# Kernel tuning notes

Hardware: AMD Instinct MI355X
Metric: run time of the kernel (lower is better)

Reference implementation:

```python
import jax, jax.numpy as jnp
import numpy as np

EPS = 1e-08
NEG_WEIGHT = 0.5
B, D = 4096, 256


def setup_inputs() -> dict:
    key = jax.random.key(0)
    k1, k2 = jax.random.split(key)
    feature_a = jax.random.normal(k1, (B, D), dtype=jnp.float32)
    feature_b = jax.random.normal(k2, (B, D), dtype=jnp.float32)
    labels = jnp.ones((B,), dtype=jnp.float32)  # positive pairs on the diagonal block
    return {"feature_a": feature_a, "feature_b": feature_b, "labels": labels}


def reference(feature_a, feature_b, labels):
    b = feature_a.shape[0]
    num_neg = b - 1
    # Cosine via single GEMM instead of the torch repeat/cat loop.
    # torch.nn.CosineSimilarity: dot / max(||a||*||b||, eps)
    na = jnp.sqrt(jnp.sum(feature_a * feature_a, axis=1))  # [B]
    nb = jnp.sqrt(jnp.sum(feature_b * feature_b, axis=1))  # [B]
    dots = jnp.einsum('kd,jd->kj', feature_a, feature_b)   # [B,B] dots[k,j]=a_k.b_j
    # torch ordering: block s (shift), row k pairs a_k with b_{(k+s) % B}
    k = jnp.arange(b)
    s = jnp.arange(b)
    idx = (k[None, :] + s[:, None]) % b                    # [S,K]
    cos = dots[k[None, :], idx] / jnp.maximum(na[None, :] * nb[idx], EPS)  # [S,K]
    logits = ((cos + 1.0) * 0.5).reshape(-1)               # flatten s-major (matches torch cat order)
    labels_full = jnp.concatenate(
        [labels.reshape(-1), jnp.zeros((num_neg * b,), dtype=labels.dtype)])
    weight = jnp.concatenate(
        [jnp.ones((b,), dtype=logits.dtype),
         jnp.full((num_neg * b,), NEG_WEIGHT, dtype=logits.dtype)])
    # BCELoss(weight, reduction='sum') with torch's log clamp at -100
    log_p = jnp.maximum(jnp.log(logits), -100.0)
    log_1mp = jnp.maximum(jnp.log1p(-logits), -100.0)
    loss = -jnp.sum(weight * (labels_full * log_p + (1.0 - labels_full) * log_1mp))
    return (logits, loss)
```

## Files before the change

### kernel.cpp

```cpp
#include <hip/hip_runtime.h>
#include <stdint.h>

#define NB 4096
#define ND 256

typedef __attribute__((ext_vector_type(8))) short short8;
typedef __attribute__((ext_vector_type(4))) float f32x4;

__device__ __forceinline__ unsigned short f2bf(float f) {
    unsigned int u = __float_as_uint(f);
    u += 0x7FFFu + ((u >> 16) & 1u);
    return (unsigned short)(u >> 16);
}

__device__ __forceinline__ void gload16(const void* g, void* lds_uniform) {
    __builtin_amdgcn_global_load_lds(
        (const __attribute__((address_space(1))) void*)(uintptr_t)g,
        (__attribute__((address_space(3))) void*)(unsigned int)(uintptr_t)lds_uniform,
        16, 0, 0);
}

__global__ void __launch_bounds__(256) prep_kernel(
    const float* __restrict__ A, const float* __restrict__ Bf,
    unsigned short* __restrict__ Abf, unsigned short* __restrict__ Bbf,
    float* __restrict__ rna, float* __restrict__ rnb, float* __restrict__ lossws)
{
    if (blockIdx.x == 0 && threadIdx.x < 64) lossws[threadIdx.x << 5] = 0.0f;
    int gw   = (blockIdx.x * 256 + threadIdx.x) >> 6;
    int lane = threadIdx.x & 63;
    const float* src; unsigned short* dst; float* rn; int row;
    if (gw < NB) { src = A;  dst = Abf; rn = rna; row = gw; }
    else         { src = Bf; dst = Bbf; rn = rnb; row = gw - NB; }

    float4 v = reinterpret_cast<const float4*>(src + (size_t)row * ND)[lane];
    float ss = v.x * v.x + v.y * v.y + v.z * v.z + v.w * v.w;
    #pragma unroll
    for (int off = 32; off > 0; off >>= 1) ss += __shfl_down(ss, off);
    if (lane == 0) rn[row] = 1.0f / sqrtf(fmaxf(ss, 1e-30f));

    ushort4 u;
    u.x = f2bf(v.x); u.y = f2bf(v.y); u.z = f2bf(v.z); u.w = f2bf(v.w);
    reinterpret_cast<ushort4*>(dst + (size_t)row * ND)[lane] = u;
}

__global__ void __launch_bounds__(256, 6) gemm_kernel(
    const unsigned short* __restrict__ Abf, const unsigned short* __restrict__ Bbf,
    const float* __restrict__ rna, const float* __restrict__ rnb,
    const float* __restrict__ labels, float* __restrict__ out,
    float* __restrict__ lossws)
{
    __shared__ __align__(16) char smem[24576];

    const int tid = threadIdx.x;
    const int w = tid >> 6, lane = tid & 63;
    const int lane15 = lane & 15, lhi = lane >> 4;
    const int bk = blockIdx.x & 63, bs = blockIdx.x >> 6;
    const int k0 = bk << 6, s0 = bs << 6;
    const int j0 = (k0 + s0) & (NB - 1);

    f32x4 acc[5];
    #pragma unroll
    for (int r = 0; r < 5; ++r) acc[r] = (f32x4)0.0f;

    auto stage = [&](int kt, char* buf) {
        {
            int slot0 = w << 6;
            int slot  = slot0 + lane;
            int row   = slot >> 2;
            int sch   = (slot ^ (slot >> 2) ^ (slot >> 4)) & 3;
            gload16(Abf + (size_t)(k0 + row) * ND + (kt << 5) + (sch << 3), buf + slot0 * 16);
        }
        #pragma unroll
        for (int i = 0; i < 2; ++i) {
            int slot0 = (i << 8) + (w << 6);
            int slot  = slot0 + lane;
            int row   = slot >> 2;
            int srow  = (j0 + row) & (NB - 1);
            int sch   = (slot ^ (slot >> 2) ^ (slot >> 4)) & 3;
            gload16(Bbf + (size_t)srow * ND + (kt << 5) + (sch << 3), buf + 4096 + slot0 * 16);
        }
    };

    stage(0, smem);
    __syncthreads();

    for (int kt = 0; kt < 8; ++kt) {
        char* buf = smem + ((kt & 1) ? 12288 : 0);
        if (kt < 7) stage(kt + 1, smem + ((kt & 1) ? 0 : 12288));
        const int f = (lane15 ^ (lane15 >> 2)) & 3;
        short8 af;
        {
            int row = (w << 4) + lane15;
            af = *reinterpret_cast<const short8*>(buf + row * 64 + ((lhi ^ f) << 4));
        }
        #pragma unroll
        for (int r = 0; r < 5; ++r) {
            int brow = (w << 4) + (r << 4) + lane15;
            short8 bfr = *reinterpret_cast<const short8*>(buf + 4096 + brow * 64 + ((lhi ^ f) << 4));
            acc[r] = __builtin_amdgcn_mfma_f32_16x16x32_bf16(af, bfr, acc[r], 0, 0, 0);
        }
        __syncthreads();
    }

    float* dw      = reinterpret_cast<float*>(smem);
    float* rnb_lds = reinterpret_cast<float*>(smem + 16384);
    float* rna_lds = reinterpret_cast<float*>(smem + 16896);
    float* lpart   = reinterpret_cast<float*>(smem + 17152);

    if (tid < 128) rnb_lds[tid] = rnb[(j0 + tid) & (NB - 1)];
    if (tid < 64)  rna_lds[tid] = rna[k0 + tid];

    #pragma unroll
    for (int r = 0; r < 5; ++r)
        #pragma unroll
        for (int e = 0; e < 4; ++e) {
            int t = (r << 4) + lane15 - (lhi << 2) - e;
            if ((unsigned)t < 64u) {
                int kap = (w << 4) + (lhi << 2) + e;
                dw[(t << 6) + (kap ^ ((t & 7) << 2))] = acc[r][e];
            }
        }
    __syncthreads();

    const int trow = (w << 4) + (lane >> 2);
    const int g0 = lane & 3;
    const int s = s0 + trow;
    float lacc = 0.0f;
    #pragma unroll
    for (int i = 0; i < 4; ++i) {
        int lg = (i << 2) + g0;
        int pg = lg ^ (trow & 7);
        f32x4 d  = *reinterpret_cast<f32x4*>(dw + (trow << 6) + (pg << 2));
        f32x4 na = *reinterpret_cast<f32x4*>(rna_lds + (lg << 2));
        f32x4 x;
        #pragma unroll
        for (int e = 0; e < 4; ++e) {
            float rb = rnb_lds[(lg << 2) + e + trow];
            x[e] = fmaf(d[e] * na[e] * rb, 0.5f, 0.5f);
        }
        *reinterpret_cast<f32x4*>(out + (size_t)s * NB + k0 + (lg << 2)) = x;
        float l1p0 = fmaxf(__logf(1.0f - x[0]), -100.0f);
        float l1p1 = fmaxf(__logf(1.0f - x[1]), -100.0f);
        float l1p2 = fmaxf(__logf(1.0f - x[2]), -100.0f);
        float l1p3 = fmaxf(__logf(1.0f - x[3]), -100.0f);
        if (s == 0) {
            float l1pv[4] = {l1p0, l1p1, l1p2, l1p3};
            #pragma unroll
            for (int e = 0; e < 4; ++e) {
                float lab = labels[k0 + (lg << 2) + e];
                float lp  = fmaxf(__logf(x[e]), -100.0f);
                lacc += lab * lp + (1.0f - lab) * l1pv[e];
            }
        } else {
            lacc += 0.5f * (l1p0 + l1p1 + l1p2 + l1p3);
        }
    }

    #pragma unroll
    for (int off = 32; off > 0; off >>= 1) lacc += __shfl_down(lacc, off);
    if (lane == 0) lpart[w] = lacc;
    __syncthreads();
    if (tid == 0) {
        float tot = lpart[0] + lpart[1] + lpart[2] + lpart[3];
        atomicAdd(lossws + ((blockIdx.x & 63) << 5), -tot);
    }
}

__global__ void finalize_kernel(const float* __restrict__ lossws, float* __restrict__ out) {
    float s = 0.0f;
    for (int i = 0; i < 64; ++i) s += lossws[i << 5];
    out[(size_t)NB * NB] = s;
}

extern "C" void kernel_launch(void* const* d_in, const int* in_sizes, int n_in,
                              void* d_out, int out_size, void* d_ws, size_t ws_size,
                              hipStream_t stream) {
    (void)in_sizes; (void)n_in; (void)out_size; (void)ws_size;
    const float* A      = (const float*)d_in[0];
    const float* Bf     = (const float*)d_in[1];
    const float* labels = (const float*)d_in[2];
    float* out = (float*)d_out;

    char* ws = (char*)d_ws;
    unsigned short* Abf = (unsigned short*)ws;
    unsigned short* Bbf = (unsigned short*)(ws + (size_t)2 * 1024 * 1024);
    float* rna    = (float*)(ws + (size_t)4 * 1024 * 1024);
    float* rnb    = (float*)(ws + (size_t)4 * 1024 * 1024 + 16384);
    float* lossws = (float*)(ws + (size_t)4 * 1024 * 1024 + 32768);

    hipLaunchKernelGGL(prep_kernel, dim3(2048), dim3(256), 0, stream,
                       A, Bf, Abf, Bbf, rna, rnb, lossws);
    hipLaunchKernelGGL(gemm_kernel, dim3(4096), dim3(256), 0, stream,
                       Abf, Bbf, rna, rnb, labels, out, lossws);
    hipLaunchKernelGGL(finalize_kernel, dim3(1), dim3(1), 0, stream, lossws, out);
}
```

Baseline: 47.93 us.

## Pre-normalize rows in prep and load MFMA operands directly from global

The prep kernel now scales each row by its inverse norm before converting to bf16, so the GEMM epilogue no longer loads or multiplies by per-row norms. The GEMM drops the LDS double-buffered staging and instead has each wave read its MFMA fragments straight from global memory (L2). Each wave now computes a 32-row k slice, and each block covers 128 k columns, which halves the grid. The epilogue is rewritten with a new swizzled LDS transpose and a lane permutation. Normalizing before the bf16 rounding slightly changes numerics, and the direct global loads depend on cache hits rather than on explicit reuse through LDS.

```diff
diff --git a/kernel.cpp b/kernel.cpp
--- a/kernel.cpp
+++ b/kernel.cpp
@@ -13,141 +13,127 @@
     return (unsigned short)(u >> 16);
 }
 
-__device__ __forceinline__ void gload16(const void* g, void* lds_uniform) {
-    __builtin_amdgcn_global_load_lds(
-        (const __attribute__((address_space(1))) void*)(uintptr_t)g,
-        (__attribute__((address_space(3))) void*)(unsigned int)(uintptr_t)lds_uniform,
-        16, 0, 0);
-}
-
 __global__ void __launch_bounds__(256) prep_kernel(
     const float* __restrict__ A, const float* __restrict__ Bf,
     unsigned short* __restrict__ Abf, unsigned short* __restrict__ Bbf,
-    float* __restrict__ rna, float* __restrict__ rnb, float* __restrict__ lossws)
+    float* __restrict__ lossws)
 {
     if (blockIdx.x == 0 && threadIdx.x < 64) lossws[threadIdx.x << 5] = 0.0f;
     int gw   = (blockIdx.x * 256 + threadIdx.x) >> 6;
     int lane = threadIdx.x & 63;
-    const float* src; unsigned short* dst; float* rn; int row;
-    if (gw < NB) { src = A;  dst = Abf; rn = rna; row = gw; }
-    else         { src = Bf; dst = Bbf; rn = rnb; row = gw - NB; }
+    const float* src; unsigned short* dst; int row;
+    if (gw < NB) { src = A;  dst = Abf; row = gw; }
+    else         { src = Bf; dst = Bbf; row = gw - NB; }
 
     float4 v = reinterpret_cast<const float4*>(src + (size_t)row * ND)[lane];
     float ss = v.x * v.x + v.y * v.y + v.z * v.z + v.w * v.w;
     #pragma unroll
-    for (int off = 32; off > 0; off >>= 1) ss += __shfl_down(ss, off);
-    if (lane == 0) rn[row] = 1.0f / sqrtf(fmaxf(ss, 1e-30f));
+    for (int off = 1; off < 64; off <<= 1) ss += __shfl_xor(ss, off);
+    float rn = 1.0f / sqrtf(fmaxf(ss, 1e-30f));
 
     ushort4 u;
-    u.x = f2bf(v.x); u.y = f2bf(v.y); u.z = f2bf(v.z); u.w = f2bf(v.w);
+    u.x = f2bf(v.x * rn); u.y = f2bf(v.y * rn);
+    u.z = f2bf(v.z * rn); u.w = f2bf(v.w * rn);
     reinterpret_cast<ushort4*>(dst + (size_t)row * ND)[lane] = u;
 }
 
-__global__ void __launch_bounds__(256, 6) gemm_kernel(
+__global__ void __launch_bounds__(256, 4) gemm_kernel(
     const unsigned short* __restrict__ Abf, const unsigned short* __restrict__ Bbf,
-    const float* __restrict__ rna, const float* __restrict__ rnb,
     const float* __restrict__ labels, float* __restrict__ out,
     float* __restrict__ lossws)
 {
-    __shared__ __align__(16) char smem[24576];
+    __shared__ __align__(16) float dw[64 * 128];
+    __shared__ float lpart[4];
 
     const int tid = threadIdx.x;
     const int w = tid >> 6, lane = tid & 63;
     const int lane15 = lane & 15, lhi = lane >> 4;
-    const int bk = blockIdx.x & 63, bs = blockIdx.x >> 6;
-    const int k0 = bk << 6, s0 = bs << 6;
-    const int j0 = (k0 + s0) & (NB - 1);
+    const int bk = blockIdx.x & 31, bs = blockIdx.x >> 5;
+    const int k0 = bk << 7, s0 = bs << 6;
+    const int kw = k0 + (w << 5);
 
-    f32x4 acc[5];
+    const short8* aptr[2];
+    const short8* bptr[6];
     #pragma unroll
-    for (int r = 0; r < 5; ++r) acc[r] = (f32x4)0.0f;
+    for (int m = 0; m < 2; ++m)
+        aptr[m] = reinterpret_cast<const short8*>(
+            Abf + (size_t)(kw + (m << 4) + lane15) * ND) + lhi;
+    #pragma unroll
+    for (int jf = 0; jf < 6; ++jf) {
+        int row = (kw + s0 + (jf << 4) + lane15) & (NB - 1);
+        bptr[jf] = reinterpret_cast<const short8*>(
+            Bbf + (size_t)row * ND) + lhi;
+    }
 
-    auto stage = [&](int kt, char* buf) {
-        {
-            int slot0 = w << 6;
-            int slot  = slot0 + lane;
-            int row   = slot >> 2;
-            int sch   = (slot ^ (slot >> 2) ^ (slot >> 4)) & 3;
-            gload16(Abf + (size_t)(k0 + row) * ND + (kt << 5) + (sch << 3), buf + slot0 * 16);
-        }
+    f32x4 acc[2][5];
+    #pragma unroll
+    for (int m = 0; m < 2; ++m)
         #pragma unroll
-        for (int i = 0; i < 2; ++i) {
-            int slot0 = (i << 8) + (w << 6);
-            int slot  = slot0 + lane;
-            int row   = slot >> 2;
-            int srow  = (j0 + row) & (NB - 1);
-            int sch   = (slot ^ (slot >> 2) ^ (slot >> 4)) & 3;
-            gload16(Bbf + (size_t)srow * ND + (kt << 5) + (sch << 3), buf + 4096 + slot0 * 16);
-        }
-    };
+        for (int r = 0; r < 5; ++r) acc[m][r] = (f32x4)0.0f;
 
-    stage(0, smem);
+    #pragma unroll
+    for (int ks = 0; ks < 8; ++ks) {
+        short8 a[2], b[6];
+        #pragma unroll
+        for (int m = 0; m < 2; ++m) a[m] = aptr[m][ks << 2];
+        #pragma unroll
+        for (int jf = 0; jf < 6; ++jf) b[jf] = bptr[jf][ks << 2];
+        #pragma unroll
+        for (int m = 0; m < 2; ++m)
+            #pragma unroll
+            for (int r = 0; r < 5; ++r)
+                acc[m][r] = __builtin_amdgcn_mfma_f32_16x16x32_bf16(
+                    a[m], b[m + r], acc[m][r], 0, 0, 0);
+    }
+
+    #pragma unroll
+    for (int m = 0; m < 2; ++m)
+        #pragma unroll
+        for (int r = 0; r < 5; ++r)
+            #pragma unroll
+            for (int e = 0; e < 4; ++e) {
+                int t = (r << 4) + lane15 - (lhi << 2) - e;
+                if ((unsigned)t < 64u) {
+                    int kap = (w << 5) + (m << 4) + (lhi << 2) + e;
+                    dw[(t << 7) + (kap ^ (t & 31))] = acc[m][r][e];
+                }
+            }
     __syncthreads();
 
-    for (int kt = 0; kt < 8; ++kt) {
-        char* buf = smem + ((kt & 1) ? 12288 : 0);
-        if (kt < 7) stage(kt + 1, smem + ((kt & 1) ? 0 : 12288));
-        const int f = (lane15 ^ (lane15 >> 2)) & 3;
-        short8 af;
-        {
-            int row = (w << 4) + lane15;
-            af = *reinterpret_cast<const short8*>(buf + row * 64 + ((lhi ^ f) << 4));
-        }
-        #pragma unroll
-        for (int r = 0; r < 5; ++r) {
-            int brow = (w << 4) + (r << 4) + lane15;
-            short8 bfr = *reinterpret_cast<const short8*>(buf + 4096 + brow * 64 + ((lhi ^ f) << 4));
-            acc[r] = __builtin_amdgcn_mfma_f32_16x16x32_bf16(af, bfr, acc[r], 0, 0, 0);
-        }
-        __syncthreads();
-    }
-
-    float* dw      = reinterpret_cast<float*>(smem);
-    float* rnb_lds = reinterpret_cast<float*>(smem + 16384);
-    float* rna_lds = reinterpret_cast<float*>(smem + 16896);
-    float* lpart   = reinterpret_cast<float*>(smem + 17152);
-
-    if (tid < 128) rnb_lds[tid] = rnb[(j0 + tid) & (NB - 1)];
-    if (tid < 64)  rna_lds[tid] = rna[k0 + tid];
+    const int t = w + (lane15 << 2);
+    const int s = s0 + t;
+    const int x3 = w & 3;
+    const float* rowp = dw + (t << 7);
+    float lacc = 0.0f;
 
     #pragma unroll
-    for (int r = 0; r < 5; ++r)
+    for (int i = 0; i < 8; ++i) {
+        int qlog  = lhi + (i << 2);
+        int physq = qlog ^ (lane15 & 7);
+        f32x4 d = *reinterpret_cast<const f32x4*>(rowp + (physq << 2));
+        f32x4 v;
+        if      (x3 == 0) { v = d; }
+        else if (x3 == 1) { v[0] = d[1]; v[1] = d[0]; v[2] = d[3]; v[3] = d[2]; }
+        else if (x3 == 2) { v[0] = d[2]; v[1] = d[3]; v[2] = d[0]; v[3] = d[1]; }
+        else              { v[0] = d[3]; v[1] = d[2]; v[2] = d[1]; v[3] = d[0]; }
+
+        f32x4 x, y;
         #pragma unroll
         for (int e = 0; e < 4; ++e) {
-            int t = (r << 4) + lane15 - (lhi << 2) - e;
-            if ((unsigned)t < 64u) {
-                int kap = (w << 4) + (lhi << 2) + e;
-                dw[(t << 6) + (kap ^ ((t & 7) << 2))] = acc[r][e];
-            }
+            x[e] = fmaf(v[e],  0.5f, 0.5f);
+            y[e] = fmaf(v[e], -0.5f, 0.5f);
         }
-    __syncthreads();
+        *reinterpret_cast<f32x4*>(out + (size_t)s * NB + k0 + (qlog << 2)) = x;
 
-    const int trow = (w << 4) + (lane >> 2);
-    const int g0 = lane & 3;
-    const int s = s0 + trow;
-    float lacc = 0.0f;
-    #pragma unroll
-    for (int i = 0; i < 4; ++i) {
-        int lg = (i << 2) + g0;
-        int pg = lg ^ (trow & 7);
-        f32x4 d  = *reinterpret_cast<f32x4*>(dw + (trow << 6) + (pg << 2));
-        f32x4 na = *reinterpret_cast<f32x4*>(rna_lds + (lg << 2));
-        f32x4 x;
-        #pragma unroll
-        for (int e = 0; e < 4; ++e) {
-            float rb = rnb_lds[(lg << 2) + e + trow];
-            x[e] = fmaf(d[e] * na[e] * rb, 0.5f, 0.5f);
-        }
-        *reinterpret_cast<f32x4*>(out + (size_t)s * NB + k0 + (lg << 2)) = x;
-        float l1p0 = fmaxf(__logf(1.0f - x[0]), -100.0f);
-        float l1p1 = fmaxf(__logf(1.0f - x[1]), -100.0f);
-        float l1p2 = fmaxf(__logf(1.0f - x[2]), -100.0f);
-        float l1p3 = fmaxf(__logf(1.0f - x[3]), -100.0f);
+        float l1p0 = fmaxf(__logf(y[0]), -100.0f);
+        float l1p1 = fmaxf(__logf(y[1]), -100.0f);
+        float l1p2 = fmaxf(__logf(y[2]), -100.0f);
+        float l1p3 = fmaxf(__logf(y[3]), -100.0f);
         if (s == 0) {
             float l1pv[4] = {l1p0, l1p1, l1p2, l1p3};
             #pragma unroll
             for (int e = 0; e < 4; ++e) {
-                float lab = labels[k0 + (lg << 2) + e];
+                float lab = labels[k0 + (qlog << 2) + e];
                 float lp  = fmaxf(__logf(x[e]), -100.0f);
                 lacc += lab * lp + (1.0f - lab) * l1pv[e];
             }
@@ -184,13 +170,11 @@
     char* ws = (char*)d_ws;
     unsigned short* Abf = (unsigned short*)ws;
     unsigned short* Bbf = (unsigned short*)(ws + (size_t)2 * 1024 * 1024);
-    float* rna    = (float*)(ws + (size_t)4 * 1024 * 1024);
-    float* rnb    = (float*)(ws + (size_t)4 * 1024 * 1024 + 16384);
-    float* lossws = (float*)(ws + (size_t)4 * 1024 * 1024 + 32768);
+    float* lossws = (float*)(ws + (size_t)4 * 1024 * 1024);
 
     hipLaunchKernelGGL(prep_kernel, dim3(2048), dim3(256), 0, stream,
-                       A, Bf, Abf, Bbf, rna, rnb, lossws);
-    hipLaunchKernelGGL(gemm_kernel, dim3(4096), dim3(256), 0, stream,
-                       Abf, Bbf, rna, rnb, labels, out, lossws);
+                       A, Bf, Abf, Bbf, lossws);
+    hipLaunchKernelGGL(gemm_kernel, dim3(2048), dim3(256), 0, stream,
+                       Abf, Bbf, labels, out, lossws);
     hipLaunchKernelGGL(finalize_kernel, dim3(1), dim3(1), 0, stream, lossws, out);
 }
```

Measured after the change: 77.33 us. 1.61x slower.
